# Optimization experiments

Measured on AMD Instinct MI355X. Metric: run time of the kernel, lower is better.

The kernel has to match this reference:

```python
import jax, jax.numpy as jnp
import numpy as np

MAX_LEN = 512   # static padding cap for the ragged sequences
EPS = 1e-12     # F.normalize default eps


def setup_inputs() -> dict:
    key = jax.random.key(0)
    ks = jax.random.split(key, 6)
    B, T, D, H = 2048, 262144, 64, 128
    x = jax.random.normal(ks[0], (T, D), jnp.float32)
    offsets = jnp.sort(jax.random.randint(ks[1], (B,), 0, T)).astype(jnp.int64)
    offsets = offsets.at[0].set(0)  # first segment starts at 0 as in EmbeddingLookup
    W_ih = jax.random.normal(ks[2], (3 * H, D), jnp.float32) * 0.1   # [r,z,n] stacked
    W_hh = jax.random.normal(ks[3], (3 * H, H), jnp.float32) * 0.1
    W_dense = jax.random.normal(ks[4], (D, H), jnp.float32) * 0.1
    b_dense = jax.random.normal(ks[5], (D,), jnp.float32) * 0.1
    return {"x": x, "offsets": offsets, "W_ih": W_ih, "W_hh": W_hh,
            "W_dense": W_dense, "b_dense": b_dense}


def _forward(x, W_ih, W_hh, W_dense, b_dense, offsets):
    T, D = x.shape
    B = offsets.shape[0]
    H = W_hh.shape[1]
    # segment lengths as in get_field_embedding_list: diffs + trailing segment
    lengths = jnp.concatenate([offsets[1:] - offsets[:-1], T - offsets[-1:]])
    lengths = jnp.clip(lengths, 1, MAX_LEN)
    # ragged -> padded [B, L, D] (pad_sequence equivalent)
    t_idx = jnp.arange(MAX_LEN)
    gidx = jnp.clip(offsets[:, None] + t_idx[None, :], 0, T - 1)      # [B, L]
    mask = (t_idx[None, :] < lengths[:, None]).astype(x.dtype)        # [B, L]
    padded = x[gidx] * mask[:, :, None]                               # [B, L, D]
    # single-layer GRU, bias=False, batch_first; scan over time
    xs = jnp.transpose(padded, (1, 0, 2))                             # [L, B, D]

    def step(h, x_t):
        gi = x_t @ W_ih.T                                             # [B, 3H]
        gh = h @ W_hh.T                                               # [B, 3H]
        ir, iz, inn = jnp.split(gi, 3, axis=-1)
        hr, hz, hn = jnp.split(gh, 3, axis=-1)
        r = jax.nn.sigmoid(ir + hr)
        z = jax.nn.sigmoid(iz + hz)
        n = jnp.tanh(inn + r * hn)
        h_new = (1.0 - z) * n + z * h
        return h_new, h_new

    h0 = jnp.zeros((B, H), x.dtype)
    _, ys = jax.lax.scan(step, h0, xs)                                # [L, B, H]
    gru_out = jnp.transpose(ys, (1, 0, 2))                            # [B, L, H]
    # gather_indexes: hidden state at last valid timestep
    last = gru_out[jnp.arange(B), lengths - 1]                        # [B, H]
    out = last @ W_dense.T + b_dense                                  # [B, D]
    norm = jnp.linalg.norm(out, axis=-1, keepdims=True)
    return out / jnp.maximum(norm, EPS)


def reference(x, offsets, W_ih, W_hh, W_dense, b_dense):
    return _forward(x, W_ih, W_hh, W_dense, b_dense, offsets)
```

## Files before the change

kernel.cpp:

```cpp
#include <hip/hip_runtime.h>
#include <math.h>

constexpr int D = 64;
constexpr int H = 128;
constexpr int MAXLEN = 512;
constexpr int MSEQ = 8;

typedef __attribute__((ext_vector_type(8))) short short8;
typedef __attribute__((ext_vector_type(4))) float f32x4;

__device__ __forceinline__ short f2bf(float f) {
    unsigned u = __float_as_uint(f);
    u += 0x7fffu + ((u >> 16) & 1u);
    return (short)(u >> 16);
}
__device__ __forceinline__ unsigned cvtpk(float a, float b) {
    unsigned r;
    asm volatile("v_cvt_pk_bf16_f32 %0, %1, %2" : "=v"(r) : "v"(a), "v"(b));
    return r;
}
__device__ __forceinline__ short8 pack8(float4 a, float4 b) {
    short8 r;
    r[0]=f2bf(a.x); r[1]=f2bf(a.y); r[2]=f2bf(a.z); r[3]=f2bf(a.w);
    r[4]=f2bf(b.x); r[5]=f2bf(b.y); r[6]=f2bf(b.z); r[7]=f2bf(b.w);
    return r;
}
__device__ __forceinline__ float rcp_(float x) { return __builtin_amdgcn_rcpf(x); }
__device__ __forceinline__ float sig_(float v) { return rcp_(1.0f + __expf(-v)); }
__device__ __forceinline__ float tanh_(float v) {
    float a = fabsf(v);
    float e = __expf(2.0f * a);
    float t = 1.0f - 2.0f * rcp_(e + 1.0f);
    return copysignf(t, v);
}
__device__ __forceinline__ void lgkm_barrier() {
    asm volatile("s_waitcnt lgkmcnt(0)\n\ts_barrier" ::: "memory");
}

#define MFMA(a,b,c) __builtin_amdgcn_mfma_f32_16x16x32_bf16((a),(b),(c),0,0,0)

__global__ __launch_bounds__(512, 2)
void gru_m8(const float* __restrict__ x,
            const int* __restrict__ offsets,
            const float* __restrict__ W_ih,
            const float* __restrict__ W_hh,
            const float* __restrict__ W_dense,
            const float* __restrict__ b_dense,
            float* __restrict__ out,
            int B, int T)
{
    const int bb   = blockIdx.x;
    const int tid  = threadIdx.x;
    const int w    = tid >> 6;
    const int l    = tid & 63;
    const int s    = l & 15;
    const int q    = l >> 4;
    const int sq   = s & 7;
    const int hsel = s >> 3;

    __shared__ __align__(16) short h_bf[2][MSEQ * H];
    __shared__ __align__(16) short x_bf[2][MSEQ * D];
    __shared__ int slen[MSEQ], sstart[MSEQ];
    __shared__ float h_f32[MSEQ][H];

    if (tid < MSEQ) {
        int sg = bb * MSEQ + tid;
        int st = 0, en = 1;
        if (sg < B) { st = offsets[sg]; en = (sg + 1 < B) ? offsets[sg + 1] : T; }
        int ln = en - st;
        ln = max(1, min(ln, MAXLEN));
        sstart[tid] = st; slen[tid] = ln;
    }
    ((int*)h_bf[0])[tid] = 0;
    __syncthreads();

    int nt = 1;
#pragma unroll
    for (int i = 0; i < MSEQ; ++i) nt = max(nt, slen[i]);

    short8 Wh[3][4];
    short8 Wi[3][2];
#pragma unroll
    for (int g = 0; g < 3; ++g) {
        const int grow = g * H + w * 16 + s;
        const float* ph = W_hh + (size_t)grow * H + q * 8;
#pragma unroll
        for (int kt = 0; kt < 4; ++kt)
            Wh[g][kt] = pack8(*(const float4*)(ph + kt * 32),
                              *(const float4*)(ph + kt * 32 + 4));
        const float* pi = W_ih + (size_t)grow * D + q * 8;
#pragma unroll
        for (int kt = 0; kt < 2; ++kt)
            Wi[g][kt] = pack8(*(const float4*)(pi + kt * 32),
                              *(const float4*)(pi + kt * 32 + 4));
    }

    int hoff[4], xoff[2];
#pragma unroll
    for (int kt = 0; kt < 4; ++kt) hoff[kt] = sq * 256 + (((kt * 4 + q) ^ sq) << 4);
#pragma unroll
    for (int kt = 0; kt < 2; ++kt) xoff[kt] = sq * 128 + (((kt * 4 + q) ^ sq) << 4);
    const int woff = sq * 256 + ((((2 * w) + (q >> 1)) ^ sq) << 4)
                   + ((q & 1) << 3) + (hsel << 2);

    const bool xact = (l < 32);
    const int  pxx  = l & 31;
    const int  st_x = sstart[w];
    const int  ln_x = slen[w];
    const float* xg = x + (size_t)st_x * D + pxx * 2;
    const int xwoff = w * 128 + ((((pxx >> 2) ^ w) << 4)) + ((pxx & 3) << 2);

    if (xact) {
        float2 v = *(const float2*)xg;
        *(unsigned*)((char*)x_bf[0] + xwoff) = cvtpk(v.x, v.y);
    }
    float2 xpf = {0.f, 0.f};
    if (xact) xpf = *(const float2*)(xg + (size_t)min(1, ln_x - 1) * D);

    const int ln_s = slen[sq];
    float h0 = 0.f, h1 = 0.f;

    __syncthreads();

    for (int t = 0; t < nt; ++t) {
        const int p = t & 1;
        const char* hb = (const char*)h_bf[p];
        const char* xb = (const char*)x_bf[p];

        short8 bh[4], bx[2];
#pragma unroll
        for (int kt = 0; kt < 4; ++kt) bh[kt] = *(const short8*)(hb + hoff[kt]);
#pragma unroll
        for (int kt = 0; kt < 2; ++kt) bx[kt] = *(const short8*)(xb + xoff[kt]);

        float2 xnew = {0.f, 0.f};
        if (xact) {
            const int tn = (t + 2 < ln_x) ? t + 2 : ln_x - 1;
            xnew = *(const float2*)(xg + (size_t)tn * D);
        }

        f32x4 cr = {0,0,0,0}, cz = {0,0,0,0}, ci = {0,0,0,0}, chh = {0,0,0,0};
#pragma unroll
        for (int kt = 0; kt < 2; ++kt) {
            cr = MFMA(Wi[0][kt], bx[kt], cr);
            cz = MFMA(Wi[1][kt], bx[kt], cz);
            ci = MFMA(Wi[2][kt], bx[kt], ci);
        }
#pragma unroll
        for (int kt = 0; kt < 4; ++kt) {
            cr  = MFMA(Wh[0][kt], bh[kt], cr);
            cz  = MFMA(Wh[1][kt], bh[kt], cz);
            chh = MFMA(Wh[2][kt], bh[kt], chh);
        }

        {
            float vr0 = hsel ? cr[2]  : cr[0],  vr1 = hsel ? cr[3]  : cr[1];
            float vz0 = hsel ? cz[2]  : cz[0],  vz1 = hsel ? cz[3]  : cz[1];
            float vi0 = hsel ? ci[2]  : ci[0],  vi1 = hsel ? ci[3]  : ci[1];
            float vh0 = hsel ? chh[2] : chh[0], vh1 = hsel ? chh[3] : chh[1];
            float r0 = sig_(vr0), r1 = sig_(vr1);
            float z0 = sig_(vz0), z1 = sig_(vz1);
            float n0 = tanh_(vi0 + r0 * vh0);
            float n1 = tanh_(vi1 + r1 * vh1);
            float hn0 = (1.0f - z0) * n0 + z0 * h0;
            float hn1 = (1.0f - z1) * n1 + z1 * h1;
            const bool upd = (t < ln_s);
            h0 = upd ? hn0 : h0;
            h1 = upd ? hn1 : h1;
        }

        *(unsigned*)((char*)h_bf[p ^ 1] + woff) = cvtpk(h0, h1);
        if (xact)
            *(unsigned*)((char*)x_bf[p ^ 1] + xwoff) = cvtpk(xpf.x, xpf.y);
        xpf = xnew;

        lgkm_barrier();
    }

    {
        float2 hv = { h0, h1 };
        *(float2*)&h_f32[sq][w * 16 + q * 4 + 2 * hsel] = hv;
    }
    __syncthreads();

    {
        const int s2 = tid >> 6;
        const int cb = tid & 63;
        float acc = b_dense[cb];
        const float* wd = W_dense + (size_t)cb * H;
        float a0=0.f,a1=0.f,a2=0.f,a3=0.f;
#pragma unroll
        for (int j = 0; j < H; j += 4) {
            float4 hv = *(const float4*)&h_f32[s2][j];
            float4 wv = *(const float4*)(wd + j);
            a0 += hv.x*wv.x; a1 += hv.y*wv.y; a2 += hv.z*wv.z; a3 += hv.w*wv.w;
        }
        acc += (a0 + a1) + (a2 + a3);
        float s2q = acc * acc;
#pragma unroll
        for (int off = 32; off >= 1; off >>= 1) s2q += __shfl_xor(s2q, off);
        float invn = 1.0f / fmaxf(sqrtf(s2q), 1e-12f);
        int sg = bb * MSEQ + s2;
        if (sg < B) out[(size_t)sg * D + cb] = acc * invn;
    }
}

extern "C" void kernel_launch(void* const* d_in, const int* in_sizes, int n_in,
                              void* d_out, int out_size, void* d_ws, size_t ws_size,
                              hipStream_t stream) {
    const float* x       = (const float*)d_in[0];
    const int*   offsets = (const int*)d_in[1];
    const float* W_ih    = (const float*)d_in[2];
    const float* W_hh    = (const float*)d_in[3];
    const float* W_dense = (const float*)d_in[4];
    const float* b_dense = (const float*)d_in[5];
    float*       out     = (float*)d_out;

    const int B = in_sizes[1];
    const int T = in_sizes[0] / D;
    const int grid = (B + MSEQ - 1) / MSEQ;

    gru_m8<<<grid, 512, 0, stream>>>(x, offsets, W_ih, W_hh, W_dense, b_dense, out, B, T);
}
```

Baseline: 349.4 us.

## Halve sequences per block to four and raise occupancy with MFMA priority

Processes 4 ragged sequences per block instead of 8, doubling the grid and reducing each block's loop count to the max length of fewer sequences, and requests 4 blocks per CU. Gate output selection is reworked for the 4-column layout, and s_setprio raises priority around the MFMA chain. This trades half-utilized MFMA columns and higher register pressure (possible spills under the tighter launch bound) for less padding waste and more concurrent latency hiding.

```diff
diff --git a/kernel.cpp b/kernel.cpp
--- a/kernel.cpp
+++ b/kernel.cpp
@@ -4,7 +4,7 @@
 constexpr int D = 64;
 constexpr int H = 128;
 constexpr int MAXLEN = 512;
-constexpr int MSEQ = 8;
+constexpr int MSEQ = 4;
 
 typedef __attribute__((ext_vector_type(8))) short short8;
 typedef __attribute__((ext_vector_type(4))) float f32x4;
@@ -36,11 +36,16 @@
 __device__ __forceinline__ void lgkm_barrier() {
     asm volatile("s_waitcnt lgkmcnt(0)\n\ts_barrier" ::: "memory");
 }
+__device__ __forceinline__ float sel4(f32x4 c, bool b0, bool b1) {
+    float a = b0 ? c[1] : c[0];
+    float b = b0 ? c[3] : c[2];
+    return b1 ? b : a;
+}
 
 #define MFMA(a,b,c) __builtin_amdgcn_mfma_f32_16x16x32_bf16((a),(b),(c),0,0,0)
 
-__global__ __launch_bounds__(512, 2)
-void gru_m8(const float* __restrict__ x,
+__global__ __launch_bounds__(512, 4)
+void gru_m4(const float* __restrict__ x,
             const int* __restrict__ offsets,
             const float* __restrict__ W_ih,
             const float* __restrict__ W_hh,
@@ -49,14 +54,15 @@
             float* __restrict__ out,
             int B, int T)
 {
-    const int bb   = blockIdx.x;
-    const int tid  = threadIdx.x;
-    const int w    = tid >> 6;
-    const int l    = tid & 63;
-    const int s    = l & 15;
-    const int q    = l >> 4;
-    const int sq   = s & 7;
-    const int hsel = s >> 3;
+    const int bb  = blockIdx.x;
+    const int tid = threadIdx.x;
+    const int w   = tid >> 6;
+    const int l   = tid & 63;
+    const int s   = l & 15;
+    const int q   = l >> 4;
+    const int sq  = s & 3;
+    const int j2  = s >> 2;
+    const bool jb0 = (j2 & 1) != 0, jb1 = (j2 & 2) != 0;
 
     __shared__ __align__(16) short h_bf[2][MSEQ * H];
     __shared__ __align__(16) short x_bf[2][MSEQ * D];
@@ -71,7 +77,7 @@
         ln = max(1, min(ln, MAXLEN));
         sstart[tid] = st; slen[tid] = ln;
     }
-    ((int*)h_bf[0])[tid] = 0;
+    if (tid < 256) ((int*)h_bf[0])[tid] = 0;
     __syncthreads();
 
     int nt = 1;
@@ -101,14 +107,15 @@
 #pragma unroll
     for (int kt = 0; kt < 2; ++kt) xoff[kt] = sq * 128 + (((kt * 4 + q) ^ sq) << 4);
     const int woff = sq * 256 + ((((2 * w) + (q >> 1)) ^ sq) << 4)
-                   + ((q & 1) << 3) + (hsel << 2);
-
-    const bool xact = (l < 32);
-    const int  pxx  = l & 31;
-    const int  st_x = sstart[w];
-    const int  ln_x = slen[w];
+                   + ((q & 1) << 3) + (j2 << 1);
+
+    const bool xact = (l < 16);
+    const int  xrow = w & 3;
+    const int  pxx  = ((w >> 2) << 4) + l;
+    const int  st_x = sstart[xrow];
+    const int  ln_x = slen[xrow];
     const float* xg = x + (size_t)st_x * D + pxx * 2;
-    const int xwoff = w * 128 + ((((pxx >> 2) ^ w) << 4)) + ((pxx & 3) << 2);
+    const int xwoff = xrow * 128 + (((pxx >> 2) ^ xrow) << 4) + ((pxx & 3) << 2);
 
     if (xact) {
         float2 v = *(const float2*)xg;
@@ -118,7 +125,7 @@
     if (xact) xpf = *(const float2*)(xg + (size_t)min(1, ln_x - 1) * D);
 
     const int ln_s = slen[sq];
-    float h0 = 0.f, h1 = 0.f;
+    float h0 = 0.f;
 
     __syncthreads();
 
@@ -139,6 +146,7 @@
             xnew = *(const float2*)(xg + (size_t)tn * D);
         }
 
+        __builtin_amdgcn_s_setprio(1);
         f32x4 cr = {0,0,0,0}, cz = {0,0,0,0}, ci = {0,0,0,0}, chh = {0,0,0,0};
 #pragma unroll
         for (int kt = 0; kt < 2; ++kt) {
@@ -152,24 +160,24 @@
             cz  = MFMA(Wh[1][kt], bh[kt], cz);
             chh = MFMA(Wh[2][kt], bh[kt], chh);
         }
+        __builtin_amdgcn_s_setprio(0);
 
         {
-            float vr0 = hsel ? cr[2]  : cr[0],  vr1 = hsel ? cr[3]  : cr[1];
-            float vz0 = hsel ? cz[2]  : cz[0],  vz1 = hsel ? cz[3]  : cz[1];
-            float vi0 = hsel ? ci[2]  : ci[0],  vi1 = hsel ? ci[3]  : ci[1];
-            float vh0 = hsel ? chh[2] : chh[0], vh1 = hsel ? chh[3] : chh[1];
-            float r0 = sig_(vr0), r1 = sig_(vr1);
-            float z0 = sig_(vz0), z1 = sig_(vz1);
-            float n0 = tanh_(vi0 + r0 * vh0);
-            float n1 = tanh_(vi1 + r1 * vh1);
-            float hn0 = (1.0f - z0) * n0 + z0 * h0;
-            float hn1 = (1.0f - z1) * n1 + z1 * h1;
-            const bool upd = (t < ln_s);
-            h0 = upd ? hn0 : h0;
-            h1 = upd ? hn1 : h1;
-        }
-
-        *(unsigned*)((char*)h_bf[p ^ 1] + woff) = cvtpk(h0, h1);
+            float vr = sel4(cr, jb0, jb1);
+            float vz = sel4(cz, jb0, jb1);
+            float vi = sel4(ci, jb0, jb1);
+            float vh = sel4(chh, jb0, jb1);
+            float r  = sig_(vr);
+            float z  = sig_(vz);
+            float n  = tanh_(vi + r * vh);
+            float hn = (1.0f - z) * n + z * h0;
+            h0 = (t < ln_s) ? hn : h0;
+        }
+
+        {
+            unsigned hu = cvtpk(h0, h0);
+            *(short*)((char*)h_bf[p ^ 1] + woff) = (short)hu;
+        }
         if (xact)
             *(unsigned*)((char*)x_bf[p ^ 1] + xwoff) = cvtpk(xpf.x, xpf.y);
         xpf = xnew;
@@ -177,13 +185,10 @@
         lgkm_barrier();
     }
 
-    {
-        float2 hv = { h0, h1 };
-        *(float2*)&h_f32[sq][w * 16 + q * 4 + 2 * hsel] = hv;
-    }
+    h_f32[sq][w * 16 + q * 4 + j2] = h0;
     __syncthreads();
 
-    {
+    if (tid < 256) {
         const int s2 = tid >> 6;
         const int cb = tid & 63;
         float acc = b_dense[cb];
@@ -220,5 +225,5 @@
     const int T = in_sizes[0] / D;
     const int grid = (B + MSEQ - 1) / MSEQ;
 
-    gru_m8<<<grid, 512, 0, stream>>>(x, offsets, W_ih, W_hh, W_dense, b_dense, out, B, T);
-}
+    gru_m4<<<grid, 512, 0, stream>>>(x, offsets, W_ih, W_hh, W_dense, b_dense, out, B, T);
+}
```

Result: slower. 508.3 us (+45.5%).
